# Performance work log

Measured on AMD Instinct MI355X. Metric: run time of the kernel, lower is better.

Reference implementation:

```python
import jax, jax.numpy as jnp
import numpy as np

K = 20            # neighbors
C = 21            # num_classes
P = 16            # patch_size
NROWS = 14        # img_size // patch_size
H = NROWS * P     # 224
TEMP = 1.0        # temperature


def setup_inputs() -> dict:
    key = jax.random.key(0)
    k1, k2, k3 = jax.random.split(key, 3)
    test_feature = jax.random.normal(k1, (8, 196, 384), dtype=jnp.float32)
    train_features = jax.random.normal(k2, (384, 50000), dtype=jnp.float32)
    train_labels = jax.random.randint(k3, (256, 50000), 0, C, dtype=jnp.int32)
    return {"test_feature": test_feature, "train_features": train_features,
            "train_labels": train_labels}


def reference(test_feature, train_features, train_labels):
    bs = test_feature.shape[0]
    # similarity: [bs, num_patches, N_train]
    sim = jnp.einsum('bpd,dn->bpn', test_feature, train_features)
    sim_k, idx = jax.lax.top_k(sim, K)              # [bs, 196, K]
    # gather neighbor patch labels: train_labels [P^2, N] -> [bs, 196, K, P^2]
    nb = train_labels.T[idx]
    # make_grid with nrow=NROWS, padding=0: assemble patches into [bs, K, H, H]
    nb = nb.reshape(bs, NROWS, NROWS, K, P, P)
    nb = nb.transpose(0, 3, 1, 4, 2, 5).reshape(bs, K, H, H)
    nb = nb.transpose(0, 2, 3, 1)                   # [bs, H, H, K]
    # weighted majority vote: nearest-upsample similarities 14x14 -> 224x224
    w = sim_k.reshape(bs, NROWS, NROWS, K)
    w = jnp.repeat(jnp.repeat(w, P, axis=1), P, axis=2)   # [bs, H, H, K]
    w = jax.nn.softmax(w / TEMP, axis=-1)
    # one-hot vote expressed as scatter-add over classes (same math, no
    # [bs,H,H,K,C] materialization)
    rows = jnp.arange(bs * H * H)
    vote = jnp.zeros((bs * H * H, C), dtype=w.dtype)
    vote = vote.at[rows[:, None], nb.reshape(bs * H * H, K)].add(
        w.reshape(bs * H * H, K))
    vote = vote.reshape(bs, H, H, C)
    pred = jnp.argmax(vote, axis=-1)                # [bs, H, H] int
    return pred
```

## Files before the change

kernel.cpp:

```cpp
#include <hip/hip_runtime.h>
#include <float.h>

#define N_TRAIN 50000
#define NPAD    50176
#define NBLKG   196
#define MPAD    1600
#define DDIM    384
#define M_ROWS  1568
#define KNN     20
#define K2      24
#define SELMAX  64
#define NCLS    21
#define CAPBUF  768
#define NENT    784

typedef __attribute__((ext_vector_type(8))) short bf16x8;
typedef __attribute__((ext_vector_type(4))) float f32x4;

static __device__ __forceinline__ unsigned short f2bf(float f) {
  unsigned int u = __float_as_uint(f);
  unsigned int r = (u + 0x7fffu + ((u >> 16) & 1u)) >> 16;
  return (unsigned short)r;
}
static __device__ __forceinline__ float bf2f(unsigned short h) {
  return __uint_as_float(((unsigned int)h) << 16);
}
static __device__ __forceinline__ unsigned int flip32(unsigned int u) {
  return (u & 0x80000000u) ? ~u : (u | 0x80000000u);
}

#define CSW(x, y) { unsigned int _hi = max(x, y); unsigned int _lo = min(x, y); x = _hi; y = _lo; }

__global__ __launch_bounds__(256) void transpose_labels(const int* __restrict__ labels,
                                                        unsigned char* __restrict__ labT) {
  __shared__ int tile[64][65];
  const int t  = threadIdx.x;
  const int c0 = blockIdx.x * 64;
  const int r0 = blockIdx.y * 64;
#pragma unroll
  for (int i = 0; i < 16; ++i) {
    int idx = i * 256 + t;
    int r = idx >> 6, c = idx & 63;
    int cc = c0 + c;
    tile[r][c] = (cc < N_TRAIN) ? labels[(size_t)(r0 + r) * N_TRAIN + cc] : 0;
  }
  __syncthreads();
#pragma unroll
  for (int i = 0; i < 16; ++i) {
    int idx = i * 256 + t;
    int c = idx >> 6, r = idx & 63;
    int cc = c0 + c;
    if (cc < N_TRAIN) labT[(size_t)cc * 256 + r0 + r] = (unsigned char)tile[r][c];
  }
}

__global__ __launch_bounds__(256) void conv_Apack(const float* __restrict__ test,
                                                  unsigned short* __restrict__ Apack) {
  int o = blockIdx.x * 256 + threadIdx.x;
  if (o >= (MPAD / 16) * 12 * 512) return;
  int j = o & 7;
  int l = (o >> 3) & 63;
  int kcmt = o >> 9;
  int kc = kcmt % 12, mt = kcmt / 12;
  int row = mt * 16 + (l & 15);
  int k = kc * 32 + (l >> 4) * 8 + j;
  Apack[o] = (row < M_ROWS) ? f2bf(test[(size_t)row * DDIM + k]) : (unsigned short)0;
}

__global__ __launch_bounds__(256) void trans_train_fused(const float* __restrict__ train,
                                                         unsigned short* __restrict__ Bpack,
                                                         float* __restrict__ trainT) {
  __shared__ float tile[64][65];
  const int t  = threadIdx.x;
  const int c0 = blockIdx.x * 64;
  const int r0 = blockIdx.y * 64;
#pragma unroll
  for (int i = 0; i < 16; ++i) {
    int idx = i * 256 + t;
    int r = idx >> 6, c = idx & 63;
    int cc = c0 + c;
    tile[r][c] = (cc < N_TRAIN) ? train[(size_t)(r0 + r) * N_TRAIN + cc] : 0.f;
  }
  __syncthreads();
#pragma unroll
  for (int it = 0; it < 2; ++it) {
    int u = it * 256 + t;
    int c = u & 63, koctL = u >> 6;
    int col = c0 + c;
    int koct = (r0 >> 3) + koctL;
    int kc = koct >> 2, l4 = koct & 3;
    int nt = col >> 4, l15 = col & 15;
    size_t base = ((size_t)(nt * 12 + kc) * 64 + l4 * 16 + l15) * 8;
    ushort4 h0, h1;
    h0.x = f2bf(tile[koctL * 8 + 0][c]); h0.y = f2bf(tile[koctL * 8 + 1][c]);
    h0.z = f2bf(tile[koctL * 8 + 2][c]); h0.w = f2bf(tile[koctL * 8 + 3][c]);
    h1.x = f2bf(tile[koctL * 8 + 4][c]); h1.y = f2bf(tile[koctL * 8 + 5][c]);
    h1.z = f2bf(tile[koctL * 8 + 6][c]); h1.w = f2bf(tile[koctL * 8 + 7][c]);
    *(ushort4*)&Bpack[base]     = h0;
    *(ushort4*)&Bpack[base + 4] = h1;
  }
#pragma unroll
  for (int i = 0; i < 16; ++i) {
    int idx = i * 256 + t;
    int c = idx >> 6, r = idx & 63;
    int cc = c0 + c;
    if (cc < N_TRAIN) trainT[(size_t)cc * DDIM + r0 + r] = tile[r][c];
  }
}

__global__ __launch_bounds__(256, 3) void mfma_gemm(const unsigned short* __restrict__ Apack,
                                                    const unsigned short* __restrict__ Bpack,
                                                    unsigned int* __restrict__ toplist) {
  __shared__ unsigned int ldsT[64 * 16];
  const int t = threadIdx.x;

  const int flat = blockIdx.x;
  const int xcd = flat & 7, jj = flat >> 3;
  const int wg = (xcd < 4 ? xcd * 613 : 2452 + (xcd - 4) * 612) + jj;
  const int mblk = wg % 25, nblk = wg / 25;
  const int m0 = mblk * 64, n0 = nblk * 256;

  const int wc = t >> 6, lane = t & 63;
  const int l15 = lane & 15, l4 = lane >> 4;

  const unsigned short* Ab = Apack + (size_t)(mblk * 4) * 12 * 512;
  const unsigned short* Bb = Bpack + (size_t)(nblk * 16 + wc * 4) * 12 * 512;

  f32x4 acc[4][4];
  const f32x4 zero = {0.f, 0.f, 0.f, 0.f};
#pragma unroll
  for (int f = 0; f < 4; ++f)
#pragma unroll
    for (int n = 0; n < 4; ++n) acc[f][n] = zero;

  for (int kc = 0; kc < 12; ++kc) {
    bf16x8 a[4], b[4];
#pragma unroll
    for (int f = 0; f < 4; ++f)
      a[f] = *(const bf16x8*)&Ab[((size_t)(f * 12 + kc) * 64 + lane) * 8];
#pragma unroll
    for (int n = 0; n < 4; ++n)
      b[n] = *(const bf16x8*)&Bb[((size_t)(n * 12 + kc) * 64 + lane) * 8];
#pragma unroll
    for (int f = 0; f < 4; ++f)
#pragma unroll
      for (int n = 0; n < 4; ++n)
        acc[f][n] = __builtin_amdgcn_mfma_f32_16x16x32_bf16(a[f], b[n], acc[f][n], 0, 0, 0);
  }

#pragma unroll
  for (int f = 0; f < 4; ++f) {
#pragma unroll
    for (int r = 0; r < 4; ++r) {
      const int row = f * 16 + l4 * 4 + r;
      unsigned int e[4];
#pragma unroll
      for (int n = 0; n < 4; ++n) {
        int col = n0 + wc * 64 + n * 16 + l15;
        unsigned int k16 = flip32(__float_as_uint(acc[f][n][r])) >> 16;
        e[n] = (col < N_TRAIN) ? ((k16 << 16) | (0xFFFFu - (unsigned int)col)) : 0u;
      }
      CSW(e[0], e[1]); CSW(e[2], e[3]); CSW(e[0], e[2]); CSW(e[1], e[3]); CSW(e[1], e[2]);
#pragma unroll
      for (int st = 1; st <= 8; st <<= 1) {
        unsigned int p0 = (unsigned int)__shfl_xor((int)e[0], st);
        unsigned int p1 = (unsigned int)__shfl_xor((int)e[1], st);
        unsigned int p2 = (unsigned int)__shfl_xor((int)e[2], st);
        unsigned int p3 = (unsigned int)__shfl_xor((int)e[3], st);
        unsigned int t0 = max(e[0], p3), t1 = max(e[1], p2);
        unsigned int t2 = max(e[2], p1), t3 = max(e[3], p0);
        CSW(t0, t2); CSW(t1, t3); CSW(t0, t1); CSW(t2, t3);
        e[0] = t0; e[1] = t1; e[2] = t2; e[3] = t3;
      }
      if (l15 == 0) {
        uint4 v; v.x = e[0]; v.y = e[1]; v.z = e[2]; v.w = e[3];
        *(uint4*)&ldsT[row * 16 + wc * 4] = v;
      }
    }
  }
  __syncthreads();

  if (t < 64) {
    const int grow = m0 + t;
    if (grow < M_ROWS) {
      unsigned int v[16];
#pragma unroll
      for (int q = 0; q < 4; ++q)
        *(uint4*)&v[q * 4] = *(uint4*)&ldsT[t * 16 + q * 4];
      unsigned int o0 = 0, o1 = 0, o2 = 0, o3 = 0;
#pragma unroll
      for (int j = 0; j < 16; ++j) {
        int rk = 0;
#pragma unroll
        for (int k = 0; k < 16; ++k) rk += (v[k] > v[j]) ? 1 : 0;
        if (rk == 0) o0 = v[j];
        else if (rk == 1) o1 = v[j];
        else if (rk == 2) o2 = v[j];
        else if (rk == 3) o3 = v[j];
      }
      uint4 w; w.x = o0; w.y = o1; w.z = o2; w.w = o3;
      *(uint4*)&toplist[(size_t)grow * NENT + nblk * 4] = w;
    }
  }
}

__global__ __launch_bounds__(256) void tail_fused(const unsigned int* __restrict__ toplist,
                                                  const float* __restrict__ test,
                                                  const float* __restrict__ trainT,
                                                  const unsigned char* __restrict__ labT,
                                                  int* __restrict__ out) {
  const int t = threadIdx.x, m = blockIdx.x;
  __shared__ unsigned int ent[NENT];
  __shared__ unsigned int smax[256];
  __shared__ unsigned int sbuf[CAPBUF];
  __shared__ unsigned int scnt, sTauA, sE24, ccnt2;
  __shared__ unsigned char flg[NBLKG];
  __shared__ short flist[NBLKG];
  __shared__ int fcnt, sC2;
  __shared__ unsigned int cbuf[128];
  __shared__ int    selC[SELMAX];
  __shared__ double rvs[SELMAX];
  __shared__ double sv2[SELMAX];
  __shared__ int    si2[SELMAX];
  __shared__ double earr[KNN];
  __shared__ double wv[KNN];
  __shared__ int    wi[KNN];

  if (t == 0) { scnt = 0u; fcnt = 0; ccnt2 = 0u; sC2 = 0; }
  for (int i = t; i < NENT; i += 256) ent[i] = toplist[(size_t)m * NENT + i];
  __syncthreads();

  unsigned int mx = 0u;
  for (int i = t; i < NENT; i += 256) mx = max(mx, ent[i]);
  smax[t] = mx;
  __syncthreads();
  {
    int rnk = 0;
    for (int j = 0; j < 256; ++j)
      rnk += (smax[j] > mx || (smax[j] == mx && j < t)) ? 1 : 0;
    if (rnk == K2 - 1) sTauA = mx;
  }
  __syncthreads();
  const unsigned int tauA = sTauA;

  for (int i = t; i < NENT; i += 256) {
    unsigned int e = ent[i];
    if (e >= tauA) { unsigned int p = atomicAdd(&scnt, 1u); if (p < CAPBUF) sbuf[p] = e; }
  }
  __syncthreads();
  const int C = (int)min(scnt, (unsigned int)CAPBUF);
  for (int s = t; s < C; s += 256) {
    unsigned int e = sbuf[s];
    int rk = 0;
    for (int j = 0; j < C; ++j) rk += (sbuf[j] > e) ? 1 : 0;
    if (rk == K2 - 1) sE24 = e;
  }
  __syncthreads();
  const unsigned int k24 = sE24 >> 16;

  if (t < NBLKG) {
    bool fl = (ent[t * 4 + 3] >> 16) >= k24;
    flg[t] = fl ? 1 : 0;
    if (fl) { int p = atomicAdd(&fcnt, 1); flist[p] = (short)t; }
  }
  __syncthreads();

  for (int i = t; i < NENT; i += 256) {
    unsigned int e = ent[i];
    if ((e >> 16) >= k24) {
      int col = 0xFFFF - (int)(e & 0xFFFFu);
      if (!flg[col >> 8]) { unsigned int p = atomicAdd(&ccnt2, 1u); if (p < 128) cbuf[p] = e; }
    }
  }
  __syncthreads();

  const int FC = fcnt;
  for (int q = 0; q < FC; ++q) {
    const int fb = flist[q];
    const int col = fb * 256 + t;
    if (col < N_TRAIN) {
      const float* Tc = trainT + (size_t)col * DDIM;
      const float* Tr = test + (size_t)m * DDIM;
      float s0 = 0.f;
      for (int k = 0; k < DDIM; ++k)
        s0 = fmaf(bf2f(f2bf(Tr[k])), bf2f(f2bf(Tc[k])), s0);
      unsigned int key = flip32(__float_as_uint(s0)) >> 16;
      if (key + 1u >= k24) {
        unsigned int e = (key << 16) | (0xFFFFu - (unsigned int)col);
        unsigned int p = atomicAdd(&ccnt2, 1u);
        if (p < 128) cbuf[p] = e;
      }
    }
  }
  __syncthreads();
  const int CC = (int)min(ccnt2, 128u);

  for (int s = t; s < CC; s += 256) {
    unsigned int e = cbuf[s];
    int rk = 0;
    for (int j = 0; j < CC; ++j) rk += (cbuf[j] > e) ? 1 : 0;
    if (rk < SELMAX) {
      selC[rk] = 0xFFFF - (int)(e & 0xFFFFu);
      atomicMax(&sC2, rk + 1);
    }
  }
  __syncthreads();
  const int C2 = sC2 < SELMAX ? sC2 : SELMAX;

  const int wid = t >> 6, lane = t & 63;
  float tr[DDIM / 64];
#pragma unroll
  for (int dd = 0; dd < DDIM / 64; ++dd)
    tr[dd] = test[(size_t)m * DDIM + dd * 64 + lane];
#pragma unroll 1
  for (int c = wid; c < C2; c += 4) {
    const float* Tc = trainT + (size_t)selC[c] * DDIM;
    double s = 0.0;
#pragma unroll
    for (int dd = 0; dd < DDIM / 64; ++dd)
      s += (double)tr[dd] * (double)Tc[dd * 64 + lane];
#pragma unroll
    for (int off = 32; off > 0; off >>= 1) s += __shfl_xor(s, off);
    if (lane == 0) rvs[c] = s;
  }
  __syncthreads();

  if (t < C2) {
    double v = rvs[t]; int id = selC[t];
    int r = 0;
    for (int n = 0; n < C2; ++n)
      r += (rvs[n] > v || (rvs[n] == v && selC[n] < id)) ? 1 : 0;
    sv2[r] = v; si2[r] = id;
  }
  __syncthreads();

  if (t < KNN) earr[t] = exp(sv2[t] - sv2[0]);
  __syncthreads();
  if (t < KNN) {
    double ssum = 0.0;
    for (int k = 0; k < KNN; ++k) ssum += earr[k];
    wv[t] = earr[t] / ssum;
    wi[t] = si2[t];
  }
  __syncthreads();

  unsigned int packed[5];
#pragma unroll
  for (int q = 0; q < 5; ++q) {
    unsigned int p = 0;
#pragma unroll
    for (int j = 0; j < 4; ++j)
      p |= (unsigned int)labT[(size_t)wi[q * 4 + j] * 256 + t] << (8 * j);
    packed[q] = p;
  }
  double best = -1.0; int bc = 0;
#pragma unroll 1
  for (int c = 0; c < NCLS; ++c) {
    double s = 0.0;
#pragma unroll
    for (int k = 0; k < KNN; ++k) {
      unsigned int lab = (packed[k >> 2] >> ((k & 3) * 8)) & 255u;
      s += (lab == (unsigned int)c) ? wv[k] : 0.0;
    }
    if (s > best) { best = s; bc = c; }
  }
  const int b = m / 196, p = m % 196;
  const int py = p / 14, px = p % 14;
  const int i = t >> 4, j = t & 15;
  out[((size_t)b * 224 + py * 16 + i) * 224 + px * 16 + j] = bc;
}

extern "C" void kernel_launch(void* const* d_in, const int* in_sizes, int n_in,
                              void* d_out, int out_size, void* d_ws, size_t ws_size,
                              hipStream_t stream) {
  const float* test  = (const float*)d_in[0];
  const float* train = (const float*)d_in[1];
  const int* labels  = (const int*)d_in[2];
  int* out = (int*)d_out;
  char* ws = (char*)d_ws;

  unsigned char*  labT    = (unsigned char*)ws;
  unsigned short* Apack   = (unsigned short*)(ws + 12800000);
  unsigned short* Bpack   = (unsigned short*)(ws + 14028800);
  float*          trainT  = (float*)(ws + 52563968);
  unsigned int*   toplist = (unsigned int*)(ws + 129363968);

  transpose_labels<<<dim3(782, 4), 256, 0, stream>>>(labels, labT);
  conv_Apack<<<dim3((MPAD / 16) * 12 * 512 / 256), 256, 0, stream>>>(test, Apack);
  trans_train_fused<<<dim3(784, 6), 256, 0, stream>>>(train, Bpack, trainT);
  mfma_gemm<<<dim3(25 * NBLKG), 256, 0, stream>>>(Apack, Bpack, toplist);
  tail_fused<<<dim3(M_ROWS), 256, 0, stream>>>(toplist, test, trainT, labT, out);
}
```

Baseline: 238.1 us.

## Retile GEMM to 128-row blocks with LDS-resident A and 128-column top-4 groups

The GEMM now uses 512-thread workgroups that stage a 128-row A panel into LDS once via global_load_lds and reuse it across two 512-column passes. Each wave computes a 64x128 tile and does the top-4 reduction per 128-column group, so the 16-way ranking pass in LDS is gone. This doubles the toplist width (1568 entries per row), and the tail kernel is adapted to 128-column flag blocks with a capped flag list. The aim is to cut redundant A reloads and launch count. In exchange it uses about 104 KB of LDS per block, has fewer resident waves, and the tail kernel has more entries to scan.

```diff
diff --git a/kernel.cpp b/kernel.cpp
--- a/kernel.cpp
+++ b/kernel.cpp
@@ -3,8 +3,8 @@
 
 #define N_TRAIN 50000
 #define NPAD    50176
-#define NBLKG   196
-#define MPAD    1600
+#define NBLKS   392
+#define MPAD    1664
 #define DDIM    384
 #define M_ROWS  1568
 #define KNN     20
@@ -12,10 +12,14 @@
 #define SELMAX  64
 #define NCLS    21
 #define CAPBUF  768
-#define NENT    784
+#define NENT    1568
 
 typedef __attribute__((ext_vector_type(8))) short bf16x8;
 typedef __attribute__((ext_vector_type(4))) float f32x4;
+
+#define GLOAD_LDS16(gp, lp) \
+  __builtin_amdgcn_global_load_lds((const __attribute__((address_space(1))) void*)(gp), \
+                                   (__attribute__((address_space(3))) void*)(lp), 16, 0, 0)
 
 static __device__ __forceinline__ unsigned short f2bf(float f) {
   unsigned int u = __float_as_uint(f);
@@ -108,99 +112,103 @@
   }
 }
 
-__global__ __launch_bounds__(256, 3) void mfma_gemm(const unsigned short* __restrict__ Apack,
+__global__ __launch_bounds__(512, 2) void mfma_gemm(const unsigned short* __restrict__ Apack,
                                                     const unsigned short* __restrict__ Bpack,
                                                     unsigned int* __restrict__ toplist) {
-  __shared__ unsigned int ldsT[64 * 16];
+  extern __shared__ unsigned short lds16[];
+  uint4* bounce = (uint4*)((char*)lds16 + 98304);
   const int t = threadIdx.x;
 
   const int flat = blockIdx.x;
   const int xcd = flat & 7, jj = flat >> 3;
-  const int wg = (xcd < 4 ? xcd * 613 : 2452 + (xcd - 4) * 612) + jj;
-  const int mblk = wg % 25, nblk = wg / 25;
-  const int m0 = mblk * 64, n0 = nblk * 256;
-
-  const int wc = t >> 6, lane = t & 63;
+  const int wg = (xcd < 5 ? xcd * 80 : 400 + (xcd - 5) * 79) + jj;
+  const int mblk = wg % 13, ngrp = wg / 13;
+  const int m0 = mblk * 128;
+
+  const int wid = t >> 6, lane = t & 63;
+  const int wr = wid >> 2, wc = wid & 3;
   const int l15 = lane & 15, l4 = lane >> 4;
 
-  const unsigned short* Ab = Apack + (size_t)(mblk * 4) * 12 * 512;
-  const unsigned short* Bb = Bpack + (size_t)(nblk * 16 + wc * 4) * 12 * 512;
-
-  f32x4 acc[4][4];
-  const f32x4 zero = {0.f, 0.f, 0.f, 0.f};
-#pragma unroll
-  for (int f = 0; f < 4; ++f)
-#pragma unroll
-    for (int n = 0; n < 4; ++n) acc[f][n] = zero;
-
-  for (int kc = 0; kc < 12; ++kc) {
-    bf16x8 a[4], b[4];
+  const unsigned short* Asrc = Apack + (size_t)(mblk * 8) * 12 * 512;
+#pragma unroll
+  for (int j = 0; j < 12; ++j)
+    GLOAD_LDS16(Asrc + (size_t)j * 4096 + wid * 512 + lane * 8,
+                &lds16[j * 4096 + wid * 512]);
+  __syncthreads();
+
+#pragma unroll 1
+  for (int s = 0; s < 2; ++s) {
+    const int colbase = ngrp * 1024 + s * 512;
+    const unsigned short* Bb = Bpack + (size_t)(colbase / 16 + wc * 8) * 12 * 512;
+
+    f32x4 acc[4][8];
+    const f32x4 zero = {0.f, 0.f, 0.f, 0.f};
 #pragma unroll
     for (int f = 0; f < 4; ++f)
-      a[f] = *(const bf16x8*)&Ab[((size_t)(f * 12 + kc) * 64 + lane) * 8];
-#pragma unroll
-    for (int n = 0; n < 4; ++n)
-      b[n] = *(const bf16x8*)&Bb[((size_t)(n * 12 + kc) * 64 + lane) * 8];
-#pragma unroll
-    for (int f = 0; f < 4; ++f)
-#pragma unroll
-      for (int n = 0; n < 4; ++n)
-        acc[f][n] = __builtin_amdgcn_mfma_f32_16x16x32_bf16(a[f], b[n], acc[f][n], 0, 0, 0);
-  }
-
-#pragma unroll
-  for (int f = 0; f < 4; ++f) {
-#pragma unroll
-    for (int r = 0; r < 4; ++r) {
-      const int row = f * 16 + l4 * 4 + r;
-      unsigned int e[4];
-#pragma unroll
-      for (int n = 0; n < 4; ++n) {
-        int col = n0 + wc * 64 + n * 16 + l15;
-        unsigned int k16 = flip32(__float_as_uint(acc[f][n][r])) >> 16;
-        e[n] = (col < N_TRAIN) ? ((k16 << 16) | (0xFFFFu - (unsigned int)col)) : 0u;
+#pragma unroll
+      for (int n = 0; n < 8; ++n) acc[f][n] = zero;
+
+#pragma unroll 2
+    for (int kc = 0; kc < 12; ++kc) {
+      bf16x8 a[4], b[8];
+#pragma unroll
+      for (int n = 0; n < 8; ++n)
+        b[n] = *(const bf16x8*)&Bb[((size_t)(n * 12 + kc) * 64 + lane) * 8];
+#pragma unroll
+      for (int f = 0; f < 4; ++f)
+        a[f] = *(const bf16x8*)&lds16[((wr * 4 + f) * 12 + kc) * 512 + lane * 8];
+#pragma unroll
+      for (int f = 0; f < 4; ++f)
+#pragma unroll
+        for (int n = 0; n < 8; ++n)
+          acc[f][n] = __builtin_amdgcn_mfma_f32_16x16x32_bf16(a[f], b[n], acc[f][n], 0, 0, 0);
+    }
+
+#pragma unroll
+    for (int f = 0; f < 4; ++f) {
+#pragma unroll
+      for (int r = 0; r < 4; ++r) {
+        unsigned int e[8];
+#pragma unroll
+        for (int n = 0; n < 8; ++n) {
+          int col = colbase + wc * 128 + n * 16 + l15;
+          unsigned int k16 = flip32(__float_as_uint(acc[f][n][r])) >> 16;
+          e[n] = (col < N_TRAIN) ? ((k16 << 16) | (0xFFFFu - (unsigned int)col)) : 0u;
+        }
+        CSW(e[0], e[1]); CSW(e[2], e[3]); CSW(e[0], e[2]); CSW(e[1], e[3]); CSW(e[1], e[2]);
+        CSW(e[4], e[5]); CSW(e[6], e[7]); CSW(e[4], e[6]); CSW(e[5], e[7]); CSW(e[5], e[6]);
+        unsigned int v0 = max(e[0], e[7]), v1 = max(e[1], e[6]);
+        unsigned int v2 = max(e[2], e[5]), v3 = max(e[3], e[4]);
+        CSW(v0, v2); CSW(v1, v3); CSW(v0, v1); CSW(v2, v3);
+#pragma unroll
+        for (int st = 1; st <= 8; st <<= 1) {
+          unsigned int p0 = (unsigned int)__shfl_xor((int)v0, st);
+          unsigned int p1 = (unsigned int)__shfl_xor((int)v1, st);
+          unsigned int p2 = (unsigned int)__shfl_xor((int)v2, st);
+          unsigned int p3 = (unsigned int)__shfl_xor((int)v3, st);
+          unsigned int t0 = max(v0, p3), t1 = max(v1, p2);
+          unsigned int t2 = max(v2, p1), t3 = max(v3, p0);
+          CSW(t0, t2); CSW(t1, t3); CSW(t0, t1); CSW(t2, t3);
+          v0 = t0; v1 = t1; v2 = t2; v3 = t3;
+        }
+        if (l15 == 0) {
+          uint4 w; w.x = v0; w.y = v1; w.z = v2; w.w = v3;
+          bounce[(wr * 64 + f * 16 + l4 * 4 + r) * 4 + wc] = w;
+        }
       }
-      CSW(e[0], e[1]); CSW(e[2], e[3]); CSW(e[0], e[2]); CSW(e[1], e[3]); CSW(e[1], e[2]);
-#pragma unroll
-      for (int st = 1; st <= 8; st <<= 1) {
-        unsigned int p0 = (unsigned int)__shfl_xor((int)e[0], st);
-        unsigned int p1 = (unsigned int)__shfl_xor((int)e[1], st);
-        unsigned int p2 = (unsigned int)__shfl_xor((int)e[2], st);
-        unsigned int p3 = (unsigned int)__shfl_xor((int)e[3], st);
-        unsigned int t0 = max(e[0], p3), t1 = max(e[1], p2);
-        unsigned int t2 = max(e[2], p1), t3 = max(e[3], p0);
-        CSW(t0, t2); CSW(t1, t3); CSW(t0, t1); CSW(t2, t3);
-        e[0] = t0; e[1] = t1; e[2] = t2; e[3] = t3;
+    }
+    __syncthreads();
+
+    {
+      int row = t >> 2, e = t & 3;
+      int grow = m0 + row;
+      if (grow < M_ROWS) {
+        uint4 w = bounce[row * 4 + e];
+        int blk = ngrp * 8 + s * 4 + e;
+        *(uint4*)&toplist[(size_t)grow * NENT + blk * 4] = w;
       }
-      if (l15 == 0) {
-        uint4 v; v.x = e[0]; v.y = e[1]; v.z = e[2]; v.w = e[3];
-        *(uint4*)&ldsT[row * 16 + wc * 4] = v;
-      }
-    }
-  }
-  __syncthreads();
-
-  if (t < 64) {
-    const int grow = m0 + t;
-    if (grow < M_ROWS) {
-      unsigned int v[16];
-#pragma unroll
-      for (int q = 0; q < 4; ++q)
-        *(uint4*)&v[q * 4] = *(uint4*)&ldsT[t * 16 + q * 4];
-      unsigned int o0 = 0, o1 = 0, o2 = 0, o3 = 0;
-#pragma unroll
-      for (int j = 0; j < 16; ++j) {
-        int rk = 0;
-#pragma unroll
-        for (int k = 0; k < 16; ++k) rk += (v[k] > v[j]) ? 1 : 0;
-        if (rk == 0) o0 = v[j];
-        else if (rk == 1) o1 = v[j];
-        else if (rk == 2) o2 = v[j];
-        else if (rk == 3) o3 = v[j];
-      }
-      uint4 w; w.x = o0; w.y = o1; w.z = o2; w.w = o3;
-      *(uint4*)&toplist[(size_t)grow * NENT + nblk * 4] = w;
-    }
+    }
+    __syncthreads();
   }
 }
 
@@ -214,8 +222,8 @@
   __shared__ unsigned int smax[256];
   __shared__ unsigned int sbuf[CAPBUF];
   __shared__ unsigned int scnt, sTauA, sE24, ccnt2;
-  __shared__ unsigned char flg[NBLKG];
-  __shared__ short flist[NBLKG];
+  __shared__ unsigned char flg[NBLKS];
+  __shared__ short flist[64];
   __shared__ int fcnt, sC2;
   __shared__ unsigned int cbuf[128];
   __shared__ int    selC[SELMAX];
@@ -258,10 +266,10 @@
   __syncthreads();
   const unsigned int k24 = sE24 >> 16;
 
-  if (t < NBLKG) {
-    bool fl = (ent[t * 4 + 3] >> 16) >= k24;
-    flg[t] = fl ? 1 : 0;
-    if (fl) { int p = atomicAdd(&fcnt, 1); flist[p] = (short)t; }
+  for (int i = t; i < NBLKS; i += 256) {
+    bool fl = (ent[i * 4 + 3] >> 16) >= k24;
+    flg[i] = fl ? 1 : 0;
+    if (fl) { int p = atomicAdd(&fcnt, 1); if (p < 64) flist[p] = (short)i; }
   }
   __syncthreads();
 
@@ -269,16 +277,16 @@
     unsigned int e = ent[i];
     if ((e >> 16) >= k24) {
       int col = 0xFFFF - (int)(e & 0xFFFFu);
-      if (!flg[col >> 8]) { unsigned int p = atomicAdd(&ccnt2, 1u); if (p < 128) cbuf[p] = e; }
-    }
-  }
-  __syncthreads();
-
-  const int FC = fcnt;
+      if (!flg[col >> 7]) { unsigned int p = atomicAdd(&ccnt2, 1u); if (p < 128) cbuf[p] = e; }
+    }
+  }
+  __syncthreads();
+
+  const int FC = min(fcnt, 64);
   for (int q = 0; q < FC; ++q) {
     const int fb = flist[q];
-    const int col = fb * 256 + t;
-    if (col < N_TRAIN) {
+    const int col = fb * 128 + t;
+    if (t < 128 && col < N_TRAIN) {
       const float* Tc = trainT + (size_t)col * DDIM;
       const float* Tr = test + (size_t)m * DDIM;
       float s0 = 0.f;
@@ -381,13 +389,13 @@
 
   unsigned char*  labT    = (unsigned char*)ws;
   unsigned short* Apack   = (unsigned short*)(ws + 12800000);
-  unsigned short* Bpack   = (unsigned short*)(ws + 14028800);
-  float*          trainT  = (float*)(ws + 52563968);
-  unsigned int*   toplist = (unsigned int*)(ws + 129363968);
+  unsigned short* Bpack   = (unsigned short*)(ws + 14077952);
+  float*          trainT  = (float*)(ws + 52613120);
+  unsigned int*   toplist = (unsigned int*)(ws + 129413120);
 
   transpose_labels<<<dim3(782, 4), 256, 0, stream>>>(labels, labT);
   conv_Apack<<<dim3((MPAD / 16) * 12 * 512 / 256), 256, 0, stream>>>(test, Apack);
   trans_train_fused<<<dim3(784, 6), 256, 0, stream>>>(train, Bpack, trainT);
-  mfma_gemm<<<dim3(25 * NBLKG), 256, 0, stream>>>(Apack, Bpack, toplist);
+  mfma_gemm<<<dim3(637), 512, 106496, stream>>>(Apack, Bpack, toplist);
   tail_fused<<<dim3(M_ROWS), 256, 0, stream>>>(toplist, test, trainT, labT, out);
 }
```

New measurement: 234.1 us. No clear change (-1.7%).
